# Kernel optimization log

Measured on AMD Instinct MI355X. Metric: run time of the kernel, lower is better.

Reference implementation:

```python
import jax, jax.numpy as jnp
import numpy as np

B, L, D_IN, D, P, NL = 8, 4096, 64, 512, 512, 3
EPS = 1e-5


def _ln(x, w, b):
    m = x.mean(-1, keepdims=True)
    v = ((x - m) ** 2).mean(-1, keepdims=True)
    return (x - m) * jax.lax.rsqrt(v + EPS) * w + b


def _gelu(x):
    return jax.nn.gelu(x, approximate=False)  # torch default = exact erf GELU


def _s5_scan(u, lam_re, lam_im, Bre, Bim, Cre, Cim, Dp, log_step):
    # u: (L, D). Diagonal complex SSM with ZOH discretization.
    lam = lam_re + 1j * lam_im                      # (P,)
    step = jnp.exp(log_step)                        # (P,)
    lam_bar = jnp.exp(lam * step)                   # (P,)
    Bt = Bre + 1j * Bim                             # (P, D)
    B_bar = ((lam_bar - 1.0) / lam)[:, None] * Bt   # (P, D)
    Bu = u.astype(jnp.complex64) @ B_bar.T          # (L, P)
    A = jnp.broadcast_to(lam_bar, Bu.shape)         # (L, P)

    def binop(a, b):
        A1, b1 = a
        A2, b2 = b
        return (A2 * A1, A2 * b1 + b2)

    _, xs = jax.lax.associative_scan(binop, (A, Bu))  # (L, P) states
    Ct = Cre + 1j * Cim                               # (D, P)
    return 2.0 * jnp.real(xs @ Ct.T) + Dp * u          # (L, D)


def setup_inputs() -> dict:
    key = jax.random.key(0)
    ks = iter(jax.random.split(key, 32))
    r = lambda s, sc=1.0: sc * jax.random.normal(next(ks), s, dtype=jnp.float32)
    inp = {}
    inp['x'] = r((B, L, D_IN))
    inp['lengths'] = jax.random.randint(next(ks), (B,), 1, L + 1, dtype=jnp.int32)
    inp['enc_w'] = r((D_IN, D), 0.05)
    inp['enc_b'] = jnp.zeros((D,), jnp.float32)
    # S5 SSM params per layer (stacked over NL)
    inp['lam_re'] = -jnp.exp(r((NL, P), 0.5))          # stable: Re(Lambda) < 0
    inp['lam_im'] = np.pi * r((NL, P))
    inp['Bre'] = r((NL, P, D), 1.0 / np.sqrt(D))
    inp['Bim'] = r((NL, P, D), 1.0 / np.sqrt(D))
    inp['Cre'] = r((NL, D, P), 1.0 / np.sqrt(P))
    inp['Cim'] = r((NL, D, P), 1.0 / np.sqrt(P))
    inp['Dp'] = r((NL, D))
    inp['log_step'] = jax.random.uniform(next(ks), (NL, P), jnp.float32, np.log(1e-3), np.log(1e-1))
    # S5Block norms and GEGLU FFN (ff_enc: D->2D no bias, ff_dec: D->D no bias)
    inp['an_w'] = jnp.ones((NL, D), jnp.float32)
    inp['an_b'] = jnp.zeros((NL, D), jnp.float32)
    inp['fn_w'] = jnp.ones((NL, D), jnp.float32)
    inp['fn_b'] = jnp.zeros((NL, D), jnp.float32)
    inp['ffe_w'] = r((NL, 2 * D, D), 1.0 / np.sqrt(D))
    inp['ffd_w'] = r((NL, D, D), 1.0 / np.sqrt(D))
    # outer prenorm LayerNorms
    inp['norm_w'] = jnp.ones((NL, D), jnp.float32)
    inp['norm_b'] = jnp.zeros((NL, D), jnp.float32)
    inp['head_w'] = r((1, D), 0.05)
    inp['head_b'] = jnp.zeros((1,), jnp.float32)
    return inp


def reference(x, lengths, enc_w, enc_b, lam_re, lam_im, Bre, Bim, Cre, Cim, Dp,
              log_step, an_w, an_b, fn_w, fn_b, ffe_w, ffd_w, norm_w, norm_b,
              head_w, head_b):
    h = x @ enc_w + enc_b  # (B, L, D)
    s5_b = jax.vmap(_s5_scan, in_axes=(0, None, None, None, None, None, None, None, None))
    for i in range(NL):
        z = _ln(h, norm_w[i], norm_b[i])  # prenorm (dropout = identity in eval)
        # --- S5Block ---
        fx = _ln(z, an_w[i], an_b[i])
        z = _gelu(s5_b(fx, lam_re[i], lam_im[i], Bre[i], Bim[i], Cre[i], Cim[i], Dp[i], log_step[i])) + fx
        fx = _ln(z, fn_w[i], fn_b[i])
        e = fx @ ffe_w[i].T                      # (B, L, 2D)
        a, g = jnp.split(e, 2, axis=-1)
        z = (a * _gelu(g)) @ ffd_w[i].T + fx      # GEGLU + residual
        h = h + z
    mask = (jnp.arange(L)[None, :] < lengths[:, None])[..., None]  # (B, L, 1)
    pooled = (h * mask).sum(axis=1) / jnp.maximum(lengths, 1)[:, None].astype(h.dtype)
    return (pooled @ head_w.T + head_b).squeeze(-1)  # (B,)
```

## Files before the change

### kernel.cpp

```cpp
#include <hip/hip_runtime.h>
#include <hip/hip_bf16.h>
#include <stdint.h>

#define BB 8
#define LL 4096
#define D_IN 64
#define DD 512
#define PP 512
#define NL 3
#define MTOK (BB * LL)
#define SCHUNK 128
#define NCHUNK (LL / SCHUNK)

typedef __bf16 bf16x8 __attribute__((ext_vector_type(8)));
typedef __bf16 bf16x4 __attribute__((ext_vector_type(4)));
typedef float f32x4 __attribute__((ext_vector_type(4)));

typedef const __attribute__((address_space(1))) void gvoid_t;
typedef __attribute__((address_space(3))) void svoid_t;

__device__ __forceinline__ void async16(const __bf16* g, __bf16* l) {
    __builtin_amdgcn_global_load_lds((gvoid_t*)g, (svoid_t*)l, 16, 0, 0);
}

__device__ __forceinline__ float gelu_f(float x) {
    return 0.5f * x * (1.0f + erff(x * 0.70710678118654752440f));
}
__device__ __forceinline__ float wred(float v) {
#pragma unroll
    for (int o = 32; o > 0; o >>= 1) v += __shfl_xor(v, o, 64);
    return v;
}
__device__ __forceinline__ float bflo(uint32_t u) { return __builtin_bit_cast(float, (uint32_t)(u << 16)); }
__device__ __forceinline__ float bfhi(uint32_t u) { return __builtin_bit_cast(float, (uint32_t)(u & 0xffff0000u)); }
__device__ __forceinline__ uint32_t packbf2(float a, float b) {
    unsigned short ha = __builtin_bit_cast(unsigned short, (__bf16)a);
    unsigned short hb = __builtin_bit_cast(unsigned short, (__bf16)b);
    return (uint32_t)ha | ((uint32_t)hb << 16);
}
__device__ __forceinline__ float ldf(const void* p, long i, int f) {
    return f ? ((const float*)p)[i] : (float)((const __bf16*)p)[i];
}
__device__ __forceinline__ void split1(float v, __bf16& h, __bf16& l) {
    h = (__bf16)v;
    l = (__bf16)(v - (float)h);
}

__global__ void detect(const uint32_t* __restrict__ an_w_raw, int* __restrict__ flag) {
    if (threadIdx.x == 0) *flag = (an_w_raw[0] == 0x3F800000u) ? 1 : 0;
}

template <int MODE>
__global__ __launch_bounds__(256) void gemm_bt(
    const __bf16* __restrict__ Ah, const __bf16* __restrict__ Al, int lda,
    const __bf16* __restrict__ Bh, const __bf16* __restrict__ Bl,
    int M, int N, int K,
    __bf16* outh, __bf16* outl, float* h32,
    __bf16* fxh, __bf16* fxl, const float* __restrict__ vec)
{
    __shared__ __attribute__((aligned(16))) char smem[35840];
    __bf16* sAh = (__bf16*)smem;
    __bf16* sAl = (__bf16*)(smem + 8192);
    __bf16* sBh = (__bf16*)(smem + 16384);
    __bf16* sBl = (__bf16*)(smem + 24576);

    const int tid = threadIdx.x;
    const int lane = tid & 63;
    const int wave = tid >> 6;
    const int wm = wave & 1, wn = wave >> 1;
    const long m0 = (long)blockIdx.x * 128;
    const long n0 = (long)blockIdx.y * 128;

    f32x4 acc[4][4] = {};

    const int sr = lane >> 2;
    const int sc = (lane & 3) * 8;
    const long ga = (m0 + wave * 32 + sr) * (long)lda + sc;
    const long gb = (n0 + wave * 32 + sr) * (long)K + sc;
    __bf16* dAh = sAh + wave * 1024;
    __bf16* dAl = sAl + wave * 1024;
    __bf16* dBh = sBh + wave * 1024;
    __bf16* dBl = sBl + wave * 1024;

    const int fr = lane & 15;
    const int fq = (lane >> 4) * 8;

    for (int k0 = 0; k0 < K; k0 += 32) {
        async16(Ah + ga + k0, dAh);
        async16(Ah + ga + k0 + 16 * (long)lda, dAh + 512);
        async16(Al + ga + k0, dAl);
        async16(Al + ga + k0 + 16 * (long)lda, dAl + 512);
        async16(Bh + gb + k0, dBh);
        async16(Bh + gb + k0 + 16 * (long)K, dBh + 512);
        async16(Bl + gb + k0, dBl);
        async16(Bl + gb + k0 + 16 * (long)K, dBl + 512);
        __syncthreads();
        bf16x8 afh[4], afl[4], bfh[4], bfl[4];
#pragma unroll
        for (int i = 0; i < 4; i++) {
            afh[i] = *(const bf16x8*)(sAh + (wm * 64 + i * 16 + fr) * 32 + fq);
            afl[i] = *(const bf16x8*)(sAl + (wm * 64 + i * 16 + fr) * 32 + fq);
            bfh[i] = *(const bf16x8*)(sBh + (wn * 64 + i * 16 + fr) * 32 + fq);
            bfl[i] = *(const bf16x8*)(sBl + (wn * 64 + i * 16 + fr) * 32 + fq);
        }
#pragma unroll
        for (int i = 0; i < 4; i++)
#pragma unroll
            for (int j = 0; j < 4; j++) {
                acc[i][j] = __builtin_amdgcn_mfma_f32_16x16x32_bf16(afh[i], bfl[j], acc[i][j], 0, 0, 0);
                acc[i][j] = __builtin_amdgcn_mfma_f32_16x16x32_bf16(afl[i], bfh[j], acc[i][j], 0, 0, 0);
                acc[i][j] = __builtin_amdgcn_mfma_f32_16x16x32_bf16(afh[i], bfh[j], acc[i][j], 0, 0, 0);
            }
        __syncthreads();
    }

    float* scratch = (float*)(smem + wave * 8960);
    const int er = (lane >> 4) * 4;
    const int ec = lane & 15;
    const int lr_rd = lane >> 3;
    const int lc_rd = (lane & 7) * 8;

#pragma unroll
    for (int g = 0; g < 2; g++) {
#pragma unroll
        for (int ii = 0; ii < 2; ii++) {
            const int i = 2 * g + ii;
#pragma unroll
            for (int j = 0; j < 4; j++)
#pragma unroll
                for (int r = 0; r < 4; r++)
                    scratch[(ii * 16 + er + r) * 68 + j * 16 + ec] = acc[i][j][r];
        }
        __syncthreads();
#pragma unroll
        for (int s = 0; s < 4; s++) {
            const int lr = s * 8 + lr_rd;
            float v8[8];
            *(f32x4*)v8       = *(const f32x4*)&scratch[lr * 68 + lc_rd];
            *(f32x4*)(v8 + 4) = *(const f32x4*)&scratch[lr * 68 + lc_rd + 4];
            const long gm = m0 + wm * 64 + g * 32 + lr;
            const int gc = (int)n0 + wn * 64 + lc_rd;
            if (MODE == 0) {
                const long idx = gm * N + gc;
                bf16x8 h8, l8;
#pragma unroll
                for (int e = 0; e < 8; e++) { __bf16 h, l; split1(v8[e], h, l); h8[e] = h; l8[e] = l; }
                *(bf16x8*)(outh + idx) = h8;
                *(bf16x8*)(outl + idx) = l8;
            } else if (MODE == 1) {
                const long idx = gm * N + gc;
                f32x4 o0, o1;
#pragma unroll
                for (int e = 0; e < 4; e++) { o0[e] = v8[e] + vec[gc + e]; o1[e] = v8[4 + e] + vec[gc + 4 + e]; }
                *(f32x4*)(h32 + idx) = o0;
                *(f32x4*)(h32 + idx + 4) = o1;
            } else if (MODE == 2) {
                const long idx = gm * N + gc;
                const bf16x8 uh = *(const bf16x8*)(fxh + idx);
                const bf16x8 ul = *(const bf16x8*)(fxl + idx);
                bf16x8 h8, l8;
#pragma unroll
                for (int e = 0; e < 8; e++) {
                    const float u = (float)uh[e] + (float)ul[e];
                    const float z = gelu_f(v8[e] + vec[gc + e] * u) + u;
                    __bf16 h, l; split1(z, h, l); h8[e] = h; l8[e] = l;
                }
                *(bf16x8*)(fxh + idx) = h8;
                *(bf16x8*)(fxl + idx) = l8;
            } else if (MODE == 3) {
                const long idx = gm * N + gc;
                const bf16x8 uh = *(const bf16x8*)(fxh + idx);
                const bf16x8 ul = *(const bf16x8*)(fxl + idx);
                f32x4 o0 = *(const f32x4*)(h32 + idx);
                f32x4 o1 = *(const f32x4*)(h32 + idx + 4);
#pragma unroll
                for (int e = 0; e < 4; e++) {
                    o0[e] += v8[e] + (float)uh[e] + (float)ul[e];
                    o1[e] += v8[4 + e] + (float)uh[4 + e] + (float)ul[4 + e];
                }
                *(f32x4*)(h32 + idx) = o0;
                *(f32x4*)(h32 + idx + 4) = o1;
            } else {
                const long tidx = gm * (N / 2) + (gc >> 1);
                bf16x4 h4, l4;
#pragma unroll
                for (int q = 0; q < 4; q++) {
                    const float t = v8[2 * q] * gelu_f(v8[2 * q + 1]);
                    __bf16 h, l; split1(t, h, l); h4[q] = h; l4[q] = l;
                }
                *(bf16x4*)(outh + tidx) = h4;
                *(bf16x4*)(outl + tidx) = l4;
            }
        }
        __syncthreads();
    }
}

template <bool DBL, bool F32IN>
__global__ __launch_bounds__(256) void ln_kernel(
    const float* __restrict__ xf, const __bf16* xh, const __bf16* xl,
    __bf16* oh, __bf16* ol,
    const float* __restrict__ w1, const float* __restrict__ b1,
    const float* __restrict__ w2, const float* __restrict__ b2)
{
    const int lane = threadIdx.x & 63;
    const int wave = threadIdx.x >> 6;
    const long row = (long)blockIdx.x * 4 + wave;
    const int c0 = lane * 8;

    float v[8];
    if (F32IN) {
        const float* xp = xf + row * DD + c0;
        const float4 a = *(const float4*)xp;
        const float4 b = *(const float4*)(xp + 4);
        v[0] = a.x; v[1] = a.y; v[2] = a.z; v[3] = a.w;
        v[4] = b.x; v[5] = b.y; v[6] = b.z; v[7] = b.w;
    } else {
        const bf16x8 a = *(const bf16x8*)(xh + row * DD + c0);
        const bf16x8 b = *(const bf16x8*)(xl + row * DD + c0);
#pragma unroll
        for (int j = 0; j < 8; j++) v[j] = (float)a[j] + (float)b[j];
    }

    float s = 0.f;
#pragma unroll
    for (int j = 0; j < 8; j++) s += v[j];
    s = wred(s);
    float m = s * (1.0f / DD);
    float q = 0.f;
#pragma unroll
    for (int j = 0; j < 8; j++) { const float d = v[j] - m; q += d * d; }
    q = wred(q);
    float rstd = rsqrtf(q * (1.0f / DD) + 1e-5f);
    float y[8];
#pragma unroll
    for (int j = 0; j < 8; j++)
        y[j] = (v[j] - m) * rstd * w1[c0 + j] + b1[c0 + j];

    if (DBL) {
        s = 0.f;
#pragma unroll
        for (int j = 0; j < 8; j++) s += y[j];
        s = wred(s);
        m = s * (1.0f / DD);
        q = 0.f;
#pragma unroll
        for (int j = 0; j < 8; j++) { const float d = y[j] - m; q += d * d; }
        q = wred(q);
        rstd = rsqrtf(q * (1.0f / DD) + 1e-5f);
#pragma unroll
        for (int j = 0; j < 8; j++)
            y[j] = (y[j] - m) * rstd * w2[c0 + j] + b2[c0 + j];
    }

    bf16x8 oh8, ol8;
#pragma unroll
    for (int j = 0; j < 8; j++) { __bf16 h, l; split1(y[j], h, l); oh8[j] = h; ol8[j] = l; }
    *(bf16x8*)(oh + row * DD + c0) = oh8;
    *(bf16x8*)(ol + row * DD + c0) = ol8;
}

__global__ void prep_lam(const void* lam_re, const void* lam_im, const void* logst,
                         float2* __restrict__ lamb, float2* __restrict__ abars,
                         float2* __restrict__ coef, const int* __restrict__ flag)
{
    const int idx = blockIdx.x * 256 + threadIdx.x;
    if (idx >= NL * PP) return;
    const int f = *flag;
    const float lre = ldf(lam_re, idx, f), lim = ldf(lam_im, idx, f);
    const float st = expf(ldf(logst, idx, f));
    const float ea = expf(lre * st);
    const float ang = lim * st;
    const float br = ea * cosf(ang), bi = ea * sinf(ang);
    lamb[idx] = make_float2(br, bi);
    float ar = br, ai = bi;
#pragma unroll
    for (int q = 0; q < 7; q++) { const float t = ar * ar - ai * ai; ai = 2.f * ar * ai; ar = t; }
    abars[idx] = make_float2(ar, ai);
    const float nr = br - 1.f, ni = bi;
    const float den = lre * lre + lim * lim;
    coef[idx] = make_float2((nr * lre + ni * lim) / den, (ni * lre - nr * lim) / den);
}

__global__ void prep_w1(const void* Bre, const void* Bim, const float2* __restrict__ coef,
                        __bf16* __restrict__ W1th, __bf16* __restrict__ W1tl,
                        const int* __restrict__ flag)
{
    const long idx = (long)blockIdx.x * 256 + threadIdx.x;
    const int f = *flag;
    const long li = idx >> 18;
    const int pd = (int)(idx & ((1 << 18) - 1));
    const int p = pd >> 9, d = pd & 511;
    const float2 c = coef[li * PP + p];
    const float br = ldf(Bre, idx, f), bi = ldf(Bim, idx, f);
    const float re = c.x * br - c.y * bi;
    const float im = c.x * bi + c.y * br;
    const long base = li * (2 * PP) * DD;
    __bf16 h, l;
    split1(re, h, l); W1th[base + (long)(2 * p) * DD + d] = h; W1tl[base + (long)(2 * p) * DD + d] = l;
    split1(im, h, l); W1th[base + (long)(2 * p + 1) * DD + d] = h; W1tl[base + (long)(2 * p + 1) * DD + d] = l;
}

__global__ void prep_w2(const void* Cre, const void* Cim,
                        __bf16* __restrict__ W2th, __bf16* __restrict__ W2tl,
                        const int* __restrict__ flag)
{
    const long idx = (long)blockIdx.x * 256 + threadIdx.x;
    const int f = *flag;
    const long li = idx >> 18;
    const int dp = (int)(idx & ((1 << 18) - 1));
    const int d = dp >> 9, p = dp & 511;
    const long base = li * DD * (2 * PP);
    __bf16 h, l;
    split1(2.f * ldf(Cre, idx, f), h, l);
    W2th[base + (long)d * (2 * PP) + 2 * p] = h; W2tl[base + (long)d * (2 * PP) + 2 * p] = l;
    split1(-2.f * ldf(Cim, idx, f), h, l);
    W2th[base + (long)d * (2 * PP) + 2 * p + 1] = h; W2tl[base + (long)d * (2 * PP) + 2 * p + 1] = l;
}

__global__ void prep_enc(const void* enc_w, __bf16* __restrict__ eh, __bf16* __restrict__ el,
                         const int* __restrict__ flag)
{
    const int idx = blockIdx.x * 256 + threadIdx.x;
    const int f = *flag;
    const int n = idx >> 6, k = idx & 63;
    __bf16 h, l;
    split1(ldf(enc_w, (long)k * DD + n, f), h, l);
    eh[idx] = h; el[idx] = l;
}

__global__ void prep_ffe(const void* src, __bf16* __restrict__ dh, __bf16* __restrict__ dl,
                         const int* __restrict__ flag)
{
    const long idx = (long)blockIdx.x * 256 + threadIdx.x;
    const int f = *flag;
    const long li = idx >> 19;
    const int rc = (int)(idx & ((1 << 19) - 1));
    const int r = rc >> 9, c = rc & 511;
    const int nr = (r < 512) ? (2 * r) : (2 * (r - 512) + 1);
    __bf16 h, l;
    split1(ldf(src, idx, f), h, l);
    const long dst = li * (1 << 19) + (long)nr * 512 + c;
    dh[dst] = h; dl[dst] = l;
}

__global__ void split_arr(const void* src, __bf16* __restrict__ dh, __bf16* __restrict__ dl,
                          long n, const int* __restrict__ flag)
{
    const long idx = (long)blockIdx.x * 256 + threadIdx.x;
    if (idx >= n) return;
    __bf16 h, l;
    split1(ldf(src, idx, *flag), h, l);
    dh[idx] = h; dl[idx] = l;
}

__global__ void cvt_many(const void* nw, const void* nb, const void* aw, const void* ab,
                         const void* fw, const void* fb, const void* dp,
                         const void* eb, const void* hw, const void* hb,
                         float* __restrict__ cv, const int* __restrict__ flag)
{
    const int idx = blockIdx.x * 256 + threadIdx.x;
    const int f = *flag;
    const int NV = NL * DD;
    if (idx < NV) cv[idx] = ldf(nw, idx, f);
    else if (idx < 2 * NV) cv[idx] = ldf(nb, idx - NV, f);
    else if (idx < 3 * NV) cv[idx] = ldf(aw, idx - 2 * NV, f);
    else if (idx < 4 * NV) cv[idx] = ldf(ab, idx - 3 * NV, f);
    else if (idx < 5 * NV) cv[idx] = ldf(fw, idx - 4 * NV, f);
    else if (idx < 6 * NV) cv[idx] = ldf(fb, idx - 5 * NV, f);
    else if (idx < 7 * NV) cv[idx] = ldf(dp, idx - 6 * NV, f);
    else if (idx < 7 * NV + 512) cv[idx] = ldf(eb, idx - 7 * NV, f);
    else if (idx < 7 * NV + 1024) cv[idx] = ldf(hw, idx - 7 * NV - 512, f);
    else if (idx < 7 * NV + 1025) cv[idx] = ldf(hb, idx - 7 * NV - 1024, f);
}

__global__ __launch_bounds__(256) void scan_ends(const uint32_t* __restrict__ wh32,
                                                 const uint32_t* __restrict__ wl32,
                                                 const float2* __restrict__ lamb,
                                                 float2* __restrict__ ends)
{
    const int idx = blockIdx.x * 256 + threadIdx.x;
    const int p = idx & 511;
    const int c = (idx >> 9) & (NCHUNK - 1);
    const int b = idx >> 14;
    const float2 lb = lamb[p];
    const long base = ((long)(b * LL + c * SCHUNK)) * 512 + p;
    float sr = 0.f, si = 0.f;
    for (int j = 0; j < SCHUNK; j++) {
        const uint32_t uh = wh32[base + (long)j * 512];
        const uint32_t ul = wl32[base + (long)j * 512];
        const float br = bflo(uh) + bflo(ul);
        const float bi = bfhi(uh) + bfhi(ul);
        const float ns = fmaf(lb.x, sr, fmaf(-lb.y, si, br));
        si = fmaf(lb.x, si, fmaf(lb.y, sr, bi));
        sr = ns;
    }
    ends[((long)(b * PP + p)) * NCHUNK + c] = make_float2(sr, si);
}

__global__ __launch_bounds__(256) void scan_carry(const float2* __restrict__ abars,
                                                  float2* __restrict__ ends)
{
    const int idx = blockIdx.x * 256 + threadIdx.x;
    const int p = idx & 511;
    const float2 As = abars[p];
    float2* eb = ends + (long)idx * NCHUNK;
    float cr = 0.f, ci = 0.f;
    for (int c = 0; c < NCHUNK; c++) {
        const float2 e = eb[c];
        eb[c] = make_float2(cr, ci);
        const float nr = As.x * cr - As.y * ci + e.x;
        ci = As.x * ci + As.y * cr + e.y;
        cr = nr;
    }
}

__global__ __launch_bounds__(256) void scan_fix(uint32_t* wh32, uint32_t* wl32,
                                                const float2* __restrict__ lamb,
                                                const float2* __restrict__ ends)
{
    const int idx = blockIdx.x * 256 + threadIdx.x;
    const int p = idx & 511;
    const int c = (idx >> 9) & (NCHUNK - 1);
    const int b = idx >> 14;
    const float2 lb = lamb[p];
    const float2 carry = ends[((long)(b * PP + p)) * NCHUNK + c];
    const long base = ((long)(b * LL + c * SCHUNK)) * 512 + p;
    float sr = carry.x, si = carry.y;
    for (int j = 0; j < SCHUNK; j++) {
        const uint32_t uh = wh32[base + (long)j * 512];
        const uint32_t ul = wl32[base + (long)j * 512];
        const float br = bflo(uh) + bflo(ul);
        const float bi = bfhi(uh) + bfhi(ul);
        const float ns = fmaf(lb.x, sr, fmaf(-lb.y, si, br));
        si = fmaf(lb.x, si, fmaf(lb.y, sr, bi));
        sr = ns;
        const float hr = (float)(__bf16)sr, hi_ = (float)(__bf16)si;
        wh32[base + (long)j * 512] = packbf2(sr, si);
        wl32[base + (long)j * 512] = packbf2(sr - hr, si - hi_);
    }
}

__global__ __launch_bounds__(256) void pool1(const float* __restrict__ h32,
                                             const float* __restrict__ hw,
                                             const int* __restrict__ lengths,
                                             float* __restrict__ partials, int b0)
{
    const int b = blockIdx.y, s = blockIdx.x;
    const int len = lengths[b0 + b];
    const float* hb = h32 + ((long)b * LL + s * 64) * DD;
    float acc = 0.f;
    for (int i = threadIdx.x; i < 64 * DD; i += 256) {
        const int tt = i >> 9;
        if (s * 64 + tt < len) acc += hb[i] * hw[i & 511];
    }
    acc = wred(acc);
    __shared__ float red[4];
    const int lane = threadIdx.x & 63, wave = threadIdx.x >> 6;
    if (lane == 0) red[wave] = acc;
    __syncthreads();
    if (threadIdx.x == 0) partials[(b0 + b) * 64 + s] = red[0] + red[1] + red[2] + red[3];
}

__global__ void pool2(const float* __restrict__ partials, const int* __restrict__ lengths,
                      const float* __restrict__ hb_, void* out, const int* __restrict__ flag)
{
    const int b = threadIdx.x;
    if (b >= BB) return;
    float s = 0.f;
    for (int c = 0; c < 64; c++) s += partials[b * 64 + c];
    const int len = lengths[b] < 1 ? 1 : lengths[b];
    const float val = s / (float)len + hb_[0];
    if (*flag) ((float*)out)[b] = val;
    else ((__bf16*)out)[b] = (__bf16)val;
}

extern "C" void kernel_launch(void* const* d_in, const int* in_sizes, int n_in,
                              void* d_out, int out_size, void* d_ws, size_t ws_size,
                              hipStream_t stream)
{
    const void* x      = d_in[0];
    const int* lengths = (const int*)d_in[1];
    const void* enc_w  = d_in[2];
    const void* enc_b  = d_in[3];
    const void* lam_re = d_in[4];
    const void* lam_im = d_in[5];
    const void* Bre    = d_in[6];
    const void* Bim    = d_in[7];
    const void* Cre    = d_in[8];
    const void* Cim    = d_in[9];
    const void* Dp     = d_in[10];
    const void* logst  = d_in[11];
    const void* an_w   = d_in[12];
    const void* an_b   = d_in[13];
    const void* fn_w   = d_in[14];
    const void* fn_b   = d_in[15];
    const void* ffe    = d_in[16];
    const void* ffd    = d_in[17];
    const void* norm_w = d_in[18];
    const void* norm_b = d_in[19];
    const void* head_w = d_in[20];
    const void* head_b = d_in[21];

    char* w = (char*)d_ws;
    auto alloc = [&](size_t bytes) -> char* {
        char* r = w;
        w += (bytes + 255) & ~(size_t)255;
        return r;
    };
    int* dflag    = (int*)alloc(256);
    __bf16* W1th  = (__bf16*)alloc((size_t)NL * 2 * PP * DD * 2);
    __bf16* W1tl  = (__bf16*)alloc((size_t)NL * 2 * PP * DD * 2);
    __bf16* W2th  = (__bf16*)alloc((size_t)NL * DD * 2 * PP * 2);
    __bf16* W2tl  = (__bf16*)alloc((size_t)NL * DD * 2 * PP * 2);
    __bf16* ffeh  = (__bf16*)alloc((size_t)NL * 2 * DD * DD * 2);
    __bf16* ffel  = (__bf16*)alloc((size_t)NL * 2 * DD * DD * 2);
    __bf16* ffdh  = (__bf16*)alloc((size_t)NL * DD * DD * 2);
    __bf16* ffdl  = (__bf16*)alloc((size_t)NL * DD * DD * 2);
    __bf16* ench  = (__bf16*)alloc((size_t)DD * D_IN * 2);
    __bf16* encl  = (__bf16*)alloc((size_t)DD * D_IN * 2);
    __bf16* xh    = (__bf16*)alloc((size_t)MTOK * D_IN * 2);
    __bf16* xl    = (__bf16*)alloc((size_t)MTOK * D_IN * 2);
    float2* lamb  = (float2*)alloc((size_t)NL * PP * 8);
    float2* abars = (float2*)alloc((size_t)NL * PP * 8);
    float2* coef  = (float2*)alloc((size_t)NL * PP * 8);
    float*  cv    = (float*)alloc((size_t)(7 * NL * DD + 1025) * 4);
    float2* ends  = (float2*)alloc((size_t)BB * PP * NCHUNK * 8);
    float* partials = (float*)alloc((size_t)BB * 64 * 4);
    const size_t fixed = (size_t)(w - (char*)d_ws);

    int NB = BB;
    const size_t per_b = (size_t)LL * DD * 16;
    while (NB > 1 && fixed + (size_t)NB * per_b > ws_size) NB >>= 1;
    float* h32  = (float*)alloc((size_t)NB * LL * DD * 4);
    __bf16* fxh = (__bf16*)alloc((size_t)NB * LL * DD * 2);
    __bf16* fxl = (__bf16*)alloc((size_t)NB * LL * DD * 2);
    __bf16* wh  = (__bf16*)alloc((size_t)NB * LL * 2 * PP * 2);
    __bf16* wl  = (__bf16*)alloc((size_t)NB * LL * 2 * PP * 2);

    const float* cv_nw = cv;
    const float* cv_nb = cv + 1536;
    const float* cv_aw = cv + 3072;
    const float* cv_ab = cv + 4608;
    const float* cv_fw = cv + 6144;
    const float* cv_fb = cv + 7680;
    const float* cv_dp = cv + 9216;
    const float* cv_eb = cv + 10752;
    const float* cv_hw = cv + 11264;
    const float* cv_hb = cv + 11776;

    detect<<<1, 64, 0, stream>>>((const uint32_t*)an_w, dflag);
    cvt_many<<<(7 * NL * DD + 1025 + 255) / 256, 256, 0, stream>>>(
        norm_w, norm_b, an_w, an_b, fn_w, fn_b, Dp, enc_b, head_w, head_b, cv, dflag);
    prep_lam<<<(NL * PP + 255) / 256, 256, 0, stream>>>(lam_re, lam_im, logst,
                                                        lamb, abars, coef, dflag);
    prep_w1<<<(NL * PP * DD) / 256, 256, 0, stream>>>(Bre, Bim, coef, W1th, W1tl, dflag);
    prep_w2<<<(NL * DD * PP) / 256, 256, 0, stream>>>(Cre, Cim, W2th, W2tl, dflag);
    prep_enc<<<(DD * D_IN) / 256, 256, 0, stream>>>(enc_w, ench, encl, dflag);
    prep_ffe<<<((size_t)NL * 2 * DD * DD) / 256, 256, 0, stream>>>(ffe, ffeh, ffel, dflag);
    split_arr<<<((size_t)NL * DD * DD + 255) / 256, 256, 0, stream>>>(
        ffd, ffdh, ffdl, (long)NL * DD * DD, dflag);
    split_arr<<<((size_t)MTOK * D_IN + 255) / 256, 256, 0, stream>>>(
        x, xh, xl, (long)MTOK * D_IN, dflag);

    for (int b0 = 0; b0 < BB; b0 += NB) {
        const int M = NB * LL;
        gemm_bt<1><<<dim3(M / 128, DD / 128), 256, 0, stream>>>(
            xh + (long)b0 * LL * D_IN, xl + (long)b0 * LL * D_IN, D_IN,
            ench, encl, M, DD, D_IN, nullptr, nullptr, h32, nullptr, nullptr, cv_eb);

        for (int li = 0; li < NL; li++) {
            ln_kernel<true, true><<<M / 4, 256, 0, stream>>>(
                h32, nullptr, nullptr, fxh, fxl,
                cv_nw + li * DD, cv_nb + li * DD, cv_aw + li * DD, cv_ab + li * DD);
            gemm_bt<0><<<dim3(M / 128, (2 * PP) / 128), 256, 0, stream>>>(
                fxh, fxl, DD, W1th + (long)li * 2 * PP * DD, W1tl + (long)li * 2 * PP * DD,
                M, 2 * PP, DD, wh, wl, nullptr, nullptr, nullptr, nullptr);
            scan_ends<<<(NB * NCHUNK * PP) / 256, 256, 0, stream>>>(
                (const uint32_t*)wh, (const uint32_t*)wl, lamb + li * PP, ends);
            scan_carry<<<(NB * PP) / 256, 256, 0, stream>>>(abars + li * PP, ends);
            scan_fix<<<(NB * NCHUNK * PP) / 256, 256, 0, stream>>>(
                (uint32_t*)wh, (uint32_t*)wl, lamb + li * PP, ends);
            gemm_bt<2><<<dim3(M / 128, DD / 128), 256, 0, stream>>>(
                wh, wl, 2 * PP, W2th + (long)li * DD * 2 * PP, W2tl + (long)li * DD * 2 * PP,
                M, DD, 2 * PP, nullptr, nullptr, nullptr, fxh, fxl, cv_dp + li * DD);
            ln_kernel<false, false><<<M / 4, 256, 0, stream>>>(
                nullptr, fxh, fxl, fxh, fxl,
                cv_fw + li * DD, cv_fb + li * DD, nullptr, nullptr);
            gemm_bt<4><<<dim3(M / 128, (2 * DD) / 128), 256, 0, stream>>>(
                fxh, fxl, DD, ffeh + (long)li * 2 * DD * DD, ffel + (long)li * 2 * DD * DD,
                M, 2 * DD, DD, wh, wl, nullptr, nullptr, nullptr, nullptr);
            gemm_bt<3><<<dim3(M / 128, DD / 128), 256, 0, stream>>>(
                wh, wl, DD, ffdh + (long)li * DD * DD, ffdl + (long)li * DD * DD,
                M, DD, DD, nullptr, nullptr, h32, fxh, fxl, nullptr);
        }
        pool1<<<dim3(64, NB), 256, 0, stream>>>(h32, cv_hw, lengths, partials, b0);
    }
    pool2<<<1, 64, 0, stream>>>(partials, lengths, cv_hb, d_out, dflag);
}
```

Baseline: 2.166 ms.

## Use 32x32 MFMA tiles, fuse pooling into last GEMM, merge prep kernels

The GEMM inner loop moves from 16x16x32 to 32x32x16 bf16 MFMA instructions, with 2x2 accumulator tiles per wave and a matching epilogue layout. It aims to cut LDS fragment reads and instruction count per FLOP. The last layer's FFN-decoder GEMM now performs the masked head-weight pooling in its epilogue (new MODE 5), which removes the h32 write and the separate pool1 pass. Several small weight-prep kernels are merged to save launches. Accumulator register pressure and write-order correctness are the main risks.

```diff
diff --git a/kernel.cpp b/kernel.cpp
--- a/kernel.cpp
+++ b/kernel.cpp
@@ -15,6 +15,7 @@
 typedef __bf16 bf16x8 __attribute__((ext_vector_type(8)));
 typedef __bf16 bf16x4 __attribute__((ext_vector_type(4)));
 typedef float f32x4 __attribute__((ext_vector_type(4)));
+typedef float f32x16 __attribute__((ext_vector_type(16)));
 
 typedef const __attribute__((address_space(1))) void gvoid_t;
 typedef __attribute__((address_space(3))) void svoid_t;
@@ -56,7 +57,8 @@
     const __bf16* __restrict__ Bh, const __bf16* __restrict__ Bl,
     int M, int N, int K,
     __bf16* outh, __bf16* outl, float* h32,
-    __bf16* fxh, __bf16* fxl, const float* __restrict__ vec)
+    __bf16* fxh, __bf16* fxl, const float* __restrict__ vec,
+    const int* __restrict__ lengths, float* __restrict__ partials, int b0)
 {
     __shared__ __attribute__((aligned(16))) char smem[35840];
     __bf16* sAh = (__bf16*)smem;
@@ -71,7 +73,7 @@
     const long m0 = (long)blockIdx.x * 128;
     const long n0 = (long)blockIdx.y * 128;
 
-    f32x4 acc[4][4] = {};
+    f32x16 acc[2][2] = {};
 
     const int sr = lane >> 2;
     const int sc = (lane & 3) * 8;
@@ -82,8 +84,8 @@
     __bf16* dBh = sBh + wave * 1024;
     __bf16* dBl = sBl + wave * 1024;
 
-    const int fr = lane & 15;
-    const int fq = (lane >> 4) * 8;
+    const int frow = lane & 31;
+    const int fcol = (lane >> 5) * 8;
 
     for (int k0 = 0; k0 < K; k0 += 32) {
         async16(Ah + ga + k0, dAh);
@@ -95,42 +97,48 @@
         async16(Bl + gb + k0, dBl);
         async16(Bl + gb + k0 + 16 * (long)K, dBl + 512);
         __syncthreads();
-        bf16x8 afh[4], afl[4], bfh[4], bfl[4];
-#pragma unroll
-        for (int i = 0; i < 4; i++) {
-            afh[i] = *(const bf16x8*)(sAh + (wm * 64 + i * 16 + fr) * 32 + fq);
-            afl[i] = *(const bf16x8*)(sAl + (wm * 64 + i * 16 + fr) * 32 + fq);
-            bfh[i] = *(const bf16x8*)(sBh + (wn * 64 + i * 16 + fr) * 32 + fq);
-            bfl[i] = *(const bf16x8*)(sBl + (wn * 64 + i * 16 + fr) * 32 + fq);
+#pragma unroll
+        for (int ks = 0; ks < 2; ks++) {
+            const int co = ks * 16 + fcol;
+            bf16x8 ah[2], al[2], bh[2], bl[2];
+#pragma unroll
+            for (int t = 0; t < 2; t++) {
+                ah[t] = *(const bf16x8*)(sAh + (wm * 64 + t * 32 + frow) * 32 + co);
+                al[t] = *(const bf16x8*)(sAl + (wm * 64 + t * 32 + frow) * 32 + co);
+                bh[t] = *(const bf16x8*)(sBh + (wn * 64 + t * 32 + frow) * 32 + co);
+                bl[t] = *(const bf16x8*)(sBl + (wn * 64 + t * 32 + frow) * 32 + co);
+            }
+#pragma unroll
+            for (int ti = 0; ti < 2; ti++)
+#pragma unroll
+                for (int tj = 0; tj < 2; tj++) {
+                    acc[ti][tj] = __builtin_amdgcn_mfma_f32_32x32x16_bf16(ah[ti], bl[tj], acc[ti][tj], 0, 0, 0);
+                    acc[ti][tj] = __builtin_amdgcn_mfma_f32_32x32x16_bf16(al[ti], bh[tj], acc[ti][tj], 0, 0, 0);
+                    acc[ti][tj] = __builtin_amdgcn_mfma_f32_32x32x16_bf16(ah[ti], bh[tj], acc[ti][tj], 0, 0, 0);
+                }
         }
-#pragma unroll
-        for (int i = 0; i < 4; i++)
-#pragma unroll
-            for (int j = 0; j < 4; j++) {
-                acc[i][j] = __builtin_amdgcn_mfma_f32_16x16x32_bf16(afh[i], bfl[j], acc[i][j], 0, 0, 0);
-                acc[i][j] = __builtin_amdgcn_mfma_f32_16x16x32_bf16(afl[i], bfh[j], acc[i][j], 0, 0, 0);
-                acc[i][j] = __builtin_amdgcn_mfma_f32_16x16x32_bf16(afh[i], bfh[j], acc[i][j], 0, 0, 0);
-            }
         __syncthreads();
     }
 
     float* scratch = (float*)(smem + wave * 8960);
-    const int er = (lane >> 4) * 4;
-    const int ec = lane & 15;
+    const int cdc = lane & 31;
+    const int rbase = 4 * (lane >> 5);
     const int lr_rd = lane >> 3;
     const int lc_rd = (lane & 7) * 8;
 
+    float pacc = 0.f;
+    int lenb = 0;
+    if (MODE == 5) lenb = lengths[b0 + (int)(blockIdx.x >> 5)];
+
 #pragma unroll
     for (int g = 0; g < 2; g++) {
 #pragma unroll
-        for (int ii = 0; ii < 2; ii++) {
-            const int i = 2 * g + ii;
-#pragma unroll
-            for (int j = 0; j < 4; j++)
-#pragma unroll
-                for (int r = 0; r < 4; r++)
-                    scratch[(ii * 16 + er + r) * 68 + j * 16 + ec] = acc[i][j][r];
-        }
+        for (int tj = 0; tj < 2; tj++)
+#pragma unroll
+            for (int r = 0; r < 16; r++) {
+                const int row = (r & 3) + 8 * (r >> 2) + rbase;
+                scratch[row * 68 + tj * 32 + cdc] = acc[g][tj][r];
+            }
         __syncthreads();
 #pragma unroll
         for (int s = 0; s < 4; s++) {
@@ -167,7 +175,7 @@
                 }
                 *(bf16x8*)(fxh + idx) = h8;
                 *(bf16x8*)(fxl + idx) = l8;
-            } else if (MODE == 3) {
+            } else if (MODE == 3 || MODE == 5) {
                 const long idx = gm * N + gc;
                 const bf16x8 uh = *(const bf16x8*)(fxh + idx);
                 const bf16x8 ul = *(const bf16x8*)(fxl + idx);
@@ -178,8 +186,16 @@
                     o0[e] += v8[e] + (float)uh[e] + (float)ul[e];
                     o1[e] += v8[4 + e] + (float)uh[4 + e] + (float)ul[4 + e];
                 }
-                *(f32x4*)(h32 + idx) = o0;
-                *(f32x4*)(h32 + idx + 4) = o1;
+                if (MODE == 3) {
+                    *(f32x4*)(h32 + idx) = o0;
+                    *(f32x4*)(h32 + idx + 4) = o1;
+                } else {
+                    if ((int)(gm & (LL - 1)) < lenb) {
+#pragma unroll
+                        for (int e = 0; e < 4; e++)
+                            pacc += o0[e] * vec[gc + e] + o1[e] * vec[gc + 4 + e];
+                    }
+                }
             } else {
                 const long tidx = gm * (N / 2) + (gc >> 1);
                 bf16x4 h4, l4;
@@ -193,6 +209,17 @@
             }
         }
         __syncthreads();
+    }
+
+    if (MODE == 5) {
+        pacc = wred(pacc);
+        float* red = (float*)smem;
+        if (lane == 0) red[wave] = pacc;
+        __syncthreads();
+        if (tid == 0)
+            partials[(long)(b0 + (int)(blockIdx.x >> 5)) * 128 +
+                     (int)(blockIdx.x & 31) * 4 + (int)blockIdx.y] =
+                red[0] + red[1] + red[2] + red[3];
     }
 }
 
@@ -260,88 +287,106 @@
     *(bf16x8*)(ol + row * DD + c0) = ol8;
 }
 
-__global__ void prep_lam(const void* lam_re, const void* lam_im, const void* logst,
-                         float2* __restrict__ lamb, float2* __restrict__ abars,
-                         float2* __restrict__ coef, const int* __restrict__ flag)
+__global__ void prep_small(const void* enc_w, __bf16* __restrict__ eh, __bf16* __restrict__ el,
+                           const void* lam_re, const void* lam_im, const void* logst,
+                           float2* __restrict__ lamb, float2* __restrict__ abars,
+                           float2* __restrict__ coef,
+                           const void* nw, const void* nb, const void* aw, const void* ab,
+                           const void* fw, const void* fb, const void* dp,
+                           const void* eb, const void* hw, const void* hb,
+                           float* __restrict__ cv, const int* __restrict__ flag)
 {
     const int idx = blockIdx.x * 256 + threadIdx.x;
-    if (idx >= NL * PP) return;
     const int f = *flag;
-    const float lre = ldf(lam_re, idx, f), lim = ldf(lam_im, idx, f);
-    const float st = expf(ldf(logst, idx, f));
-    const float ea = expf(lre * st);
-    const float ang = lim * st;
-    const float br = ea * cosf(ang), bi = ea * sinf(ang);
-    lamb[idx] = make_float2(br, bi);
-    float ar = br, ai = bi;
-#pragma unroll
-    for (int q = 0; q < 7; q++) { const float t = ar * ar - ai * ai; ai = 2.f * ar * ai; ar = t; }
-    abars[idx] = make_float2(ar, ai);
-    const float nr = br - 1.f, ni = bi;
-    const float den = lre * lre + lim * lim;
-    coef[idx] = make_float2((nr * lre + ni * lim) / den, (ni * lre - nr * lim) / den);
-}
-
-__global__ void prep_w1(const void* Bre, const void* Bim, const float2* __restrict__ coef,
-                        __bf16* __restrict__ W1th, __bf16* __restrict__ W1tl,
-                        const int* __restrict__ flag)
+    {
+        const int n = idx >> 6, k = idx & 63;
+        __bf16 h, l;
+        split1(ldf(enc_w, (long)k * DD + n, f), h, l);
+        eh[idx] = h; el[idx] = l;
+    }
+    if (idx < NL * PP) {
+        const float lre = ldf(lam_re, idx, f), lim = ldf(lam_im, idx, f);
+        const float st = expf(ldf(logst, idx, f));
+        const float ea = expf(lre * st);
+        const float ang = lim * st;
+        const float br = ea * cosf(ang), bi = ea * sinf(ang);
+        lamb[idx] = make_float2(br, bi);
+        float ar = br, ai = bi;
+#pragma unroll
+        for (int q = 0; q < 7; q++) { const float t = ar * ar - ai * ai; ai = 2.f * ar * ai; ar = t; }
+        abars[idx] = make_float2(ar, ai);
+        const float nr = br - 1.f, ni = bi;
+        const float den = lre * lre + lim * lim;
+        coef[idx] = make_float2((nr * lre + ni * lim) / den, (ni * lre - nr * lim) / den);
+    }
+    const int NV = NL * DD;
+    if (idx < 7 * NV + 1025) {
+        if (idx < NV) cv[idx] = ldf(nw, idx, f);
+        else if (idx < 2 * NV) cv[idx] = ldf(nb, idx - NV, f);
+        else if (idx < 3 * NV) cv[idx] = ldf(aw, idx - 2 * NV, f);
+        else if (idx < 4 * NV) cv[idx] = ldf(ab, idx - 3 * NV, f);
+        else if (idx < 5 * NV) cv[idx] = ldf(fw, idx - 4 * NV, f);
+        else if (idx < 6 * NV) cv[idx] = ldf(fb, idx - 5 * NV, f);
+        else if (idx < 7 * NV) cv[idx] = ldf(dp, idx - 6 * NV, f);
+        else if (idx < 7 * NV + 512) cv[idx] = ldf(eb, idx - 7 * NV, f);
+        else if (idx < 7 * NV + 1024) cv[idx] = ldf(hw, idx - 7 * NV - 512, f);
+        else cv[idx] = ldf(hb, idx - 7 * NV - 1024, f);
+    }
+}
+
+__global__ void prep_w12(const void* Bre, const void* Bim, const float2* __restrict__ coef,
+                         __bf16* __restrict__ W1th, __bf16* __restrict__ W1tl,
+                         const void* Cre, const void* Cim,
+                         __bf16* __restrict__ W2th, __bf16* __restrict__ W2tl,
+                         const int* __restrict__ flag)
 {
     const long idx = (long)blockIdx.x * 256 + threadIdx.x;
     const int f = *flag;
     const long li = idx >> 18;
     const int pd = (int)(idx & ((1 << 18) - 1));
-    const int p = pd >> 9, d = pd & 511;
-    const float2 c = coef[li * PP + p];
-    const float br = ldf(Bre, idx, f), bi = ldf(Bim, idx, f);
-    const float re = c.x * br - c.y * bi;
-    const float im = c.x * bi + c.y * br;
-    const long base = li * (2 * PP) * DD;
-    __bf16 h, l;
-    split1(re, h, l); W1th[base + (long)(2 * p) * DD + d] = h; W1tl[base + (long)(2 * p) * DD + d] = l;
-    split1(im, h, l); W1th[base + (long)(2 * p + 1) * DD + d] = h; W1tl[base + (long)(2 * p + 1) * DD + d] = l;
-}
-
-__global__ void prep_w2(const void* Cre, const void* Cim,
-                        __bf16* __restrict__ W2th, __bf16* __restrict__ W2tl,
+    {
+        const int p = pd >> 9, d = pd & 511;
+        const float2 c = coef[li * PP + p];
+        const float br = ldf(Bre, idx, f), bi = ldf(Bim, idx, f);
+        const float re = c.x * br - c.y * bi;
+        const float im = c.x * bi + c.y * br;
+        const long base = li * (2 * PP) * DD;
+        __bf16 h, l;
+        split1(re, h, l); W1th[base + (long)(2 * p) * DD + d] = h; W1tl[base + (long)(2 * p) * DD + d] = l;
+        split1(im, h, l); W1th[base + (long)(2 * p + 1) * DD + d] = h; W1tl[base + (long)(2 * p + 1) * DD + d] = l;
+    }
+    {
+        const int d = pd >> 9, p = pd & 511;
+        const long base = li * DD * (2 * PP);
+        __bf16 h, l;
+        split1(2.f * ldf(Cre, idx, f), h, l);
+        W2th[base + (long)d * (2 * PP) + 2 * p] = h; W2tl[base + (long)d * (2 * PP) + 2 * p] = l;
+        split1(-2.f * ldf(Cim, idx, f), h, l);
+        W2th[base + (long)d * (2 * PP) + 2 * p + 1] = h; W2tl[base + (long)d * (2 * PP) + 2 * p + 1] = l;
+    }
+}
+
+__global__ void prep_ff(const void* ffe, __bf16* __restrict__ feh, __bf16* __restrict__ fel,
+                        const void* ffd, __bf16* __restrict__ fdh, __bf16* __restrict__ fdl,
                         const int* __restrict__ flag)
 {
     const long idx = (long)blockIdx.x * 256 + threadIdx.x;
     const int f = *flag;
-    const long li = idx >> 18;
-    const int dp = (int)(idx & ((1 << 18) - 1));
-    const int d = dp >> 9, p = dp & 511;
-    const long base = li * DD * (2 * PP);
-    __bf16 h, l;
-    split1(2.f * ldf(Cre, idx, f), h, l);
-    W2th[base + (long)d * (2 * PP) + 2 * p] = h; W2tl[base + (long)d * (2 * PP) + 2 * p] = l;
-    split1(-2.f * ldf(Cim, idx, f), h, l);
-    W2th[base + (long)d * (2 * PP) + 2 * p + 1] = h; W2tl[base + (long)d * (2 * PP) + 2 * p + 1] = l;
-}
-
-__global__ void prep_enc(const void* enc_w, __bf16* __restrict__ eh, __bf16* __restrict__ el,
-                         const int* __restrict__ flag)
-{
-    const int idx = blockIdx.x * 256 + threadIdx.x;
-    const int f = *flag;
-    const int n = idx >> 6, k = idx & 63;
-    __bf16 h, l;
-    split1(ldf(enc_w, (long)k * DD + n, f), h, l);
-    eh[idx] = h; el[idx] = l;
-}
-
-__global__ void prep_ffe(const void* src, __bf16* __restrict__ dh, __bf16* __restrict__ dl,
-                         const int* __restrict__ flag)
-{
-    const long idx = (long)blockIdx.x * 256 + threadIdx.x;
-    const int f = *flag;
-    const long li = idx >> 19;
-    const int rc = (int)(idx & ((1 << 19) - 1));
-    const int r = rc >> 9, c = rc & 511;
-    const int nr = (r < 512) ? (2 * r) : (2 * (r - 512) + 1);
-    __bf16 h, l;
-    split1(ldf(src, idx, f), h, l);
-    const long dst = li * (1 << 19) + (long)nr * 512 + c;
-    dh[dst] = h; dl[dst] = l;
+    {
+        const long li = idx >> 19;
+        const int rc = (int)(idx & ((1 << 19) - 1));
+        const int r = rc >> 9, c = rc & 511;
+        const int nr = (r < 512) ? (2 * r) : (2 * (r - 512) + 1);
+        __bf16 h, l;
+        split1(ldf(ffe, idx, f), h, l);
+        const long dst = li * (1 << 19) + (long)nr * 512 + c;
+        feh[dst] = h; fel[dst] = l;
+    }
+    if (idx < (long)NL * DD * DD) {
+        __bf16 h, l;
+        split1(ldf(ffd, idx, f), h, l);
+        fdh[idx] = h; fdl[idx] = l;
+    }
 }
 
 __global__ void split_arr(const void* src, __bf16* __restrict__ dh, __bf16* __restrict__ dl,
@@ -352,26 +397,6 @@
     __bf16 h, l;
     split1(ldf(src, idx, *flag), h, l);
     dh[idx] = h; dl[idx] = l;
-}
-
-__global__ void cvt_many(const void* nw, const void* nb, const void* aw, const void* ab,
-                         const void* fw, const void* fb, const void* dp,
-                         const void* eb, const void* hw, const void* hb,
-                         float* __restrict__ cv, const int* __restrict__ flag)
-{
-    const int idx = blockIdx.x * 256 + threadIdx.x;
-    const int f = *flag;
-    const int NV = NL * DD;
-    if (idx < NV) cv[idx] = ldf(nw, idx, f);
-    else if (idx < 2 * NV) cv[idx] = ldf(nb, idx - NV, f);
-    else if (idx < 3 * NV) cv[idx] = ldf(aw, idx - 2 * NV, f);
-    else if (idx < 4 * NV) cv[idx] = ldf(ab, idx - 3 * NV, f);
-    else if (idx < 5 * NV) cv[idx] = ldf(fw, idx - 4 * NV, f);
-    else if (idx < 6 * NV) cv[idx] = ldf(fb, idx - 5 * NV, f);
-    else if (idx < 7 * NV) cv[idx] = ldf(dp, idx - 6 * NV, f);
-    else if (idx < 7 * NV + 512) cv[idx] = ldf(eb, idx - 7 * NV, f);
-    else if (idx < 7 * NV + 1024) cv[idx] = ldf(hw, idx - 7 * NV - 512, f);
-    else if (idx < 7 * NV + 1025) cv[idx] = ldf(hb, idx - 7 * NV - 1024, f);
 }
 
 __global__ __launch_bounds__(256) void scan_ends(const uint32_t* __restrict__ wh32,
@@ -441,34 +466,13 @@
     }
 }
 
-__global__ __launch_bounds__(256) void pool1(const float* __restrict__ h32,
-                                             const float* __restrict__ hw,
-                                             const int* __restrict__ lengths,
-                                             float* __restrict__ partials, int b0)
-{
-    const int b = blockIdx.y, s = blockIdx.x;
-    const int len = lengths[b0 + b];
-    const float* hb = h32 + ((long)b * LL + s * 64) * DD;
-    float acc = 0.f;
-    for (int i = threadIdx.x; i < 64 * DD; i += 256) {
-        const int tt = i >> 9;
-        if (s * 64 + tt < len) acc += hb[i] * hw[i & 511];
-    }
-    acc = wred(acc);
-    __shared__ float red[4];
-    const int lane = threadIdx.x & 63, wave = threadIdx.x >> 6;
-    if (lane == 0) red[wave] = acc;
-    __syncthreads();
-    if (threadIdx.x == 0) partials[(b0 + b) * 64 + s] = red[0] + red[1] + red[2] + red[3];
-}
-
 __global__ void pool2(const float* __restrict__ partials, const int* __restrict__ lengths,
                       const float* __restrict__ hb_, void* out, const int* __restrict__ flag)
 {
     const int b = threadIdx.x;
     if (b >= BB) return;
     float s = 0.f;
-    for (int c = 0; c < 64; c++) s += partials[b * 64 + c];
+    for (int c = 0; c < 128; c++) s += partials[b * 128 + c];
     const int len = lengths[b] < 1 ? 1 : lengths[b];
     const float val = s / (float)len + hb_[0];
     if (*flag) ((float*)out)[b] = val;
@@ -526,7 +530,7 @@
     float2* coef  = (float2*)alloc((size_t)NL * PP * 8);
     float*  cv    = (float*)alloc((size_t)(7 * NL * DD + 1025) * 4);
     float2* ends  = (float2*)alloc((size_t)BB * PP * NCHUNK * 8);
-    float* partials = (float*)alloc((size_t)BB * 64 * 4);
+    float* partials = (float*)alloc((size_t)BB * 128 * 4);
     const size_t fixed = (size_t)(w - (char*)d_ws);
 
     int NB = BB;
@@ -550,16 +554,14 @@
     const float* cv_hb = cv + 11776;
 
     detect<<<1, 64, 0, stream>>>((const uint32_t*)an_w, dflag);
-    cvt_many<<<(7 * NL * DD + 1025 + 255) / 256, 256, 0, stream>>>(
-        norm_w, norm_b, an_w, an_b, fn_w, fn_b, Dp, enc_b, head_w, head_b, cv, dflag);
-    prep_lam<<<(NL * PP + 255) / 256, 256, 0, stream>>>(lam_re, lam_im, logst,
-                                                        lamb, abars, coef, dflag);
-    prep_w1<<<(NL * PP * DD) / 256, 256, 0, stream>>>(Bre, Bim, coef, W1th, W1tl, dflag);
-    prep_w2<<<(NL * DD * PP) / 256, 256, 0, stream>>>(Cre, Cim, W2th, W2tl, dflag);
-    prep_enc<<<(DD * D_IN) / 256, 256, 0, stream>>>(enc_w, ench, encl, dflag);
-    prep_ffe<<<((size_t)NL * 2 * DD * DD) / 256, 256, 0, stream>>>(ffe, ffeh, ffel, dflag);
-    split_arr<<<((size_t)NL * DD * DD + 255) / 256, 256, 0, stream>>>(
-        ffd, ffdh, ffdl, (long)NL * DD * DD, dflag);
+    prep_small<<<128, 256, 0, stream>>>(enc_w, ench, encl, lam_re, lam_im, logst,
+                                        lamb, abars, coef,
+                                        norm_w, norm_b, an_w, an_b, fn_w, fn_b, Dp,
+                                        enc_b, head_w, head_b, cv, dflag);
+    prep_w12<<<(NL * PP * DD) / 256, 256, 0, stream>>>(
+        Bre, Bim, coef, W1th, W1tl, Cre, Cim, W2th, W2tl, dflag);
+    prep_ff<<<((size_t)NL * 2 * DD * DD) / 256, 256, 0, stream>>>(
+        ffe, ffeh, ffel, ffd, ffdh, ffdl, dflag);
     split_arr<<<((size_t)MTOK * D_IN + 255) / 256, 256, 0, stream>>>(
         x, xh, xl, (long)MTOK * D_IN, dflag);
 
@@ -567,7 +569,8 @@
         const int M = NB * LL;
         gemm_bt<1><<<dim3(M / 128, DD / 128), 256, 0, stream>>>(
             xh + (long)b0 * LL * D_IN, xl + (long)b0 * LL * D_IN, D_IN,
-            ench, encl, M, DD, D_IN, nullptr, nullptr, h32, nullptr, nullptr, cv_eb);
+            ench, encl, M, DD, D_IN, nullptr, nullptr, h32, nullptr, nullptr, cv_eb,
+            nullptr, nullptr, 0);
 
         for (int li = 0; li < NL; li++) {
             ln_kernel<true, true><<<M / 4, 256, 0, stream>>>(
@@ -575,7 +578,8 @@
                 cv_nw + li * DD, cv_nb + li * DD, cv_aw + li * DD, cv_ab + li * DD);
             gemm_bt<0><<<dim3(M / 128, (2 * PP) / 128), 256, 0, stream>>>(
                 fxh, fxl, DD, W1th + (long)li * 2 * PP * DD, W1tl + (long)li * 2 * PP * DD,
-                M, 2 * PP, DD, wh, wl, nullptr, nullptr, nullptr, nullptr);
+                M, 2 * PP, DD, wh, wl, nullptr, nullptr, nullptr, nullptr,
+                nullptr, nullptr, 0);
             scan_ends<<<(NB * NCHUNK * PP) / 256, 256, 0, stream>>>(
                 (const uint32_t*)wh, (const uint32_t*)wl, lamb + li * PP, ends);
             scan_carry<<<(NB * PP) / 256, 256, 0, stream>>>(abars + li * PP, ends);
@@ -583,18 +587,27 @@
                 (uint32_t*)wh, (uint32_t*)wl, lamb + li * PP, ends);
             gemm_bt<2><<<dim3(M / 128, DD / 128), 256, 0, stream>>>(
                 wh, wl, 2 * PP, W2th + (long)li * DD * 2 * PP, W2tl + (long)li * DD * 2 * PP,
-                M, DD, 2 * PP, nullptr, nullptr, nullptr, fxh, fxl, cv_dp + li * DD);
+                M, DD, 2 * PP, nullptr, nullptr, nullptr, fxh, fxl, cv_dp + li * DD,
+                nullptr, nullptr, 0);
             ln_kernel<false, false><<<M / 4, 256, 0, stream>>>(
                 nullptr, fxh, fxl, fxh, fxl,
                 cv_fw + li * DD, cv_fb + li * DD, nullptr, nullptr);
             gemm_bt<4><<<dim3(M / 128, (2 * DD) / 128), 256, 0, stream>>>(
                 fxh, fxl, DD, ffeh + (long)li * 2 * DD * DD, ffel + (long)li * 2 * DD * DD,
-                M, 2 * DD, DD, wh, wl, nullptr, nullptr, nullptr, nullptr);
-            gemm_bt<3><<<dim3(M / 128, DD / 128), 256, 0, stream>>>(
-                wh, wl, DD, ffdh + (long)li * DD * DD, ffdl + (long)li * DD * DD,
-                M, DD, DD, nullptr, nullptr, h32, fxh, fxl, nullptr);
+                M, 2 * DD, DD, wh, wl, nullptr, nullptr, nullptr, nullptr,
+                nullptr, nullptr, 0);
+            if (li < NL - 1) {
+                gemm_bt<3><<<dim3(M / 128, DD / 128), 256, 0, stream>>>(
+                    wh, wl, DD, ffdh + (long)li * DD * DD, ffdl + (long)li * DD * DD,
+                    M, DD, DD, nullptr, nullptr, h32, fxh, fxl, nullptr,
+                    nullptr, nullptr, 0);
+            } else {
+                gemm_bt<5><<<dim3(M / 128, DD / 128), 256, 0, stream>>>(
+                    wh, wl, DD, ffdh + (long)li * DD * DD, ffdl + (long)li * DD * DD,
+                    M, DD, DD, nullptr, nullptr, h32, fxh, fxl, cv_hw,
+                    lengths, partials, b0);
+            }
         }
-        pool1<<<dim3(64, NB), 256, 0, stream>>>(h32, cv_hw, lengths, partials, b0);
     }
     pool2<<<1, 64, 0, stream>>>(partials, lengths, cv_hb, d_out, dflag);
 }
```

Result: no change. 2.194 ms (+1.3%).
